# Performance work log

Hardware: AMD Instinct MI355X
Metric: run time of the kernel (lower is better)

The kernel has to match this reference:

```python
import jax, jax.numpy as jnp
import numpy as np
from jax import lax

MAX_INT = 10000.0
V, T0, E, H = 100000, 20, 256, 256
T = T0 + 2          # tagset_size + 2 (start = T-2, stop = T-1)
B, S = 32, 512
H2 = H // 2


def setup_inputs() -> dict:
    key = jax.random.key(0)
    ks = jax.random.split(key, 18)
    sd = 0.08
    trans = jax.random.normal(ks[0], (T, T), jnp.float32)
    trans = trans.at[-2, :].set(-MAX_INT).at[:, -1].set(-MAX_INT)
    return {
        "X": jax.random.randint(ks[1], (B, S), 0, V, jnp.int64),
        "Y": jax.random.randint(ks[2], (B, S), 0, T0, jnp.int64),
        "emb": jax.random.normal(ks[3], (V, E), jnp.float32) * sd,
        "Wih_f": jax.random.normal(ks[4], (4 * H2, E), jnp.float32) * sd,
        "Whh_f": jax.random.normal(ks[5], (4 * H2, H2), jnp.float32) * sd,
        "bih_f": jax.random.normal(ks[6], (4 * H2,), jnp.float32) * sd,
        "bhh_f": jax.random.normal(ks[7], (4 * H2,), jnp.float32) * sd,
        "Wih_b": jax.random.normal(ks[8], (4 * H2, E), jnp.float32) * sd,
        "Whh_b": jax.random.normal(ks[9], (4 * H2, H2), jnp.float32) * sd,
        "bih_b": jax.random.normal(ks[10], (4 * H2,), jnp.float32) * sd,
        "bhh_b": jax.random.normal(ks[11], (4 * H2,), jnp.float32) * sd,
        "fcW": jax.random.normal(ks[12], (T, H), jnp.float32) * sd,
        "fcb": jax.random.normal(ks[13], (T,), jnp.float32) * sd,
        "trans": trans,
        # original draws random (h0, c0) of shape (2, seq_len, H//2) each call
        "h0": jax.random.normal(ks[14], (2, S, H2), jnp.float32),
        "c0": jax.random.normal(ks[15], (2, S, H2), jnp.float32),
    }


def _lstm_dir(x, h0, c0, Wih, Whh, bih, bhh, reverse):
    # x: [B, S, E]; scans over axis 0 (as torch LSTM with batch_first=False does here)
    def step(carry, xt):
        h, c = carry
        g = xt @ Wih.T + bih + h @ Whh.T + bhh          # [S, 4*H2]
        i, f, gg, o = jnp.split(g, 4, axis=-1)
        c2 = jax.nn.sigmoid(f) * c + jax.nn.sigmoid(i) * jnp.tanh(gg)
        h2 = jax.nn.sigmoid(o) * jnp.tanh(c2)
        return (h2, c2), h2
    xs = x[::-1] if reverse else x
    _, hs = lax.scan(step, (h0, c0), xs)
    return hs[::-1] if reverse else hs                  # [B, S, H2]


def _feats(X, emb, Wih_f, Whh_f, bih_f, bhh_f, Wih_b, Whh_b, bih_b, bhh_b,
           fcW, fcb, h0, c0):
    e = emb[X]                                           # [B, S, E]
    hf = _lstm_dir(e, h0[0], c0[0], Wih_f, Whh_f, bih_f, bhh_f, False)
    hb = _lstm_dir(e, h0[1], c0[1], Wih_b, Whh_b, bih_b, bhh_b, True)
    lstm_out = jnp.concatenate([hf, hb], axis=-1)        # [B, S, H]
    return lstm_out @ fcW.T + fcb                        # [B, S, T]


def _crf_loss(feats, Y, trans):
    # forward algorithm (log partition), vectorized over batch
    alpha0 = jnp.full((B, T), -MAX_INT, feats.dtype).at[:, -2].set(0.0)

    def step(alpha, feat_t):                             # feat_t: [B, T]
        # alpha_new[b, next] = LSE_prev(alpha[b,prev] + trans[next,prev]) + feat[b,next]
        new = jax.nn.logsumexp(alpha[:, None, :] + trans[None, :, :], axis=2) + feat_t
        return new, None

    alpha, _ = lax.scan(step, alpha0, jnp.swapaxes(feats, 0, 1))
    forward_score = jax.nn.logsumexp(alpha + trans[-1][None, :], axis=1).mean()

    # gold score
    start = jnp.full((B, 1), T - 2, Y.dtype)
    tags = jnp.concatenate([start, Y], axis=1)           # [B, S+1]
    emit = jnp.take_along_axis(feats, Y[..., None], axis=2)[..., 0].sum(axis=1)
    trans_sc = trans[tags[:, 1:], tags[:, :-1]].sum(axis=1) + trans[-1, tags[:, -1]]
    gold_score = (emit + trans_sc).mean()
    return forward_score - gold_score


def reference(X, Y, emb, Wih_f, Whh_f, bih_f, bhh_f, Wih_b, Whh_b, bih_b, bhh_b,
              fcW, fcb, trans, h0, c0):
    feats = _feats(X, emb, Wih_f, Whh_f, bih_f, bhh_f, Wih_b, Whh_b, bih_b, bhh_b,
                   fcW, fcb, h0, c0)
    score = _crf_loss(feats, Y, trans)
    return score, Y
```

## Files before the change

kernel.cpp:

```cpp
#include <hip/hip_runtime.h>
#include <hip/hip_bf16.h>
#include <stdint.h>

typedef __attribute__((ext_vector_type(8))) short short8;
typedef __attribute__((ext_vector_type(4))) float f32x4;
typedef __attribute__((ext_vector_type(4))) unsigned short ushort4v;
typedef __attribute__((ext_vector_type(4))) unsigned int uint4v;

#define NB 32
#define NS 512
#define NE 256
#define NH2 128
#define NG 512
#define NT 22

__device__ __forceinline__ unsigned short f2bf(float f) {
    union { float f; unsigned u; } v; v.f = f;
    unsigned r = v.u + 0x7fffu + ((v.u >> 16) & 1u);
    return (unsigned short)(r >> 16);
}
__device__ __forceinline__ float bf2f(unsigned short b) {
    union { unsigned u; float f; } v; v.u = ((unsigned)b) << 16;
    return v.f;
}
__device__ __forceinline__ unsigned cvt_pk_bf16(float a, float b) {
    unsigned r;
    asm("v_cvt_pk_bf16_f32 %0, %1, %2" : "=v"(r) : "v"(a), "v"(b));
    return r;
}
__device__ __forceinline__ void wg_barrier() {
    __builtin_amdgcn_sched_barrier(0);
    asm volatile("s_waitcnt lgkmcnt(0)" ::: "memory");
    __builtin_amdgcn_s_barrier();
    __builtin_amdgcn_sched_barrier(0);
}
#define GL16(gsrc, ldst)                                                              \
    __builtin_amdgcn_global_load_lds(                                                 \
        (const __attribute__((address_space(1))) unsigned int*)(gsrc),                \
        (__attribute__((address_space(3))) unsigned int*)(ldst), 16, 0, 0)

__global__ void k_pre(const int* X, const float* emb, const int* Y,
                      const float* Wih_f, const float* Wih_b,
                      const float* Whh_f, const float* Whh_b, const float* fcW,
                      unsigned short* ebf, unsigned short* Wb_ih,
                      unsigned short* Wb_hh, unsigned short* fcpad, float* out,
                      unsigned* done_cnt)
{
    int idx = blockIdx.x * blockDim.x + threadIdx.x;
    if (idx == 0) *done_cnt = 0;
    const int nEmb = NB * NS * 64;
    if (idx < nEmb) {
        int r = idx >> 6, lane = idx & 63;
        int xr = X[r];
        f32x4 v = *(const f32x4*)(emb + (size_t)xr * NE + lane * 4);
        ushort4v o;
        o[0] = f2bf(v[0]); o[1] = f2bf(v[1]); o[2] = f2bf(v[2]); o[3] = f2bf(v[3]);
        *(ushort4v*)(ebf + (size_t)r * NE + lane * 4) = o;
        return;
    }
    int j = idx - nEmb;
    const int n1 = 2 * NG * NE;
    const int n2 = 2 * NG * NH2;
    const int n3 = 2 * 32 * NH2;
    const int n4 = NB * NS;
    if (j < n1) {
        const float* src = (j < NG * NE) ? Wih_f : Wih_b;
        Wb_ih[j] = f2bf(src[j % (NG * NE)]);
    } else if (j < n1 + n2) {
        int i2 = j - n1;
        const float* src = (i2 < NG * NH2) ? Whh_f : Whh_b;
        Wb_hh[i2] = f2bf(src[i2 % (NG * NH2)]);
    } else if (j < n1 + n2 + n3) {
        int i3 = j - n1 - n2;
        int d = i3 / (32 * NH2);
        int jj = (i3 / NH2) % 32;
        int k = i3 % NH2;
        fcpad[i3] = (jj < NT) ? f2bf(fcW[jj * 256 + d * NH2 + k]) : (unsigned short)0;
    } else if (j < n1 + n2 + n3 + n4) {
        int i4 = j - n1 - n2 - n3;
        out[1 + i4] = (float)Y[i4];
    }
}

__launch_bounds__(256)
__global__ void k_xproj(const unsigned short* ebf, const unsigned short* Wb_ih,
                        const float* bih_f, const float* bhh_f,
                        const float* bih_b, const float* bhh_b,
                        unsigned short* Xp)
{
    __shared__ __align__(16) unsigned short Atile[2][128 * 64];
    __shared__ __align__(16) unsigned short Btile[2][128 * 64];
    int dir = blockIdx.z;
    int r0 = blockIdx.x * 128;
    int g0 = blockIdx.y * 128;
    int tid = threadIdx.x;
    int w = tid >> 6, lane = tid & 63;
    int wr = w >> 1, wc = w & 1;
    int lrow = lane & 15, kg = lane >> 4;
    int srow8 = lane >> 3, schunk = lane & 7;
    const float* bih = dir ? bih_b : bih_f;
    const float* bhh = dir ? bhh_b : bhh_f;
    const unsigned short* Bsrc = Wb_ih + ((size_t)dir * NG + g0) * NE;
    const unsigned short* Asrc = ebf + (size_t)r0 * NE;

#define STAGE(bufi, ks)                                                                \
    do {                                                                               \
        int k0_ = (ks) * 64;                                                           \
        _Pragma("unroll")                                                              \
        for (int i_ = 0; i_ < 4; ++i_) {                                               \
            int rr_ = (w * 4 + i_) * 8 + srow8;                                        \
            GL16(Asrc + (size_t)rr_ * NE + k0_ + schunk * 8, &Atile[bufi][(w * 4 + i_) * 512]); \
            GL16(Bsrc + (size_t)rr_ * NE + k0_ + schunk * 8, &Btile[bufi][(w * 4 + i_) * 512]); \
        }                                                                              \
    } while (0)

    STAGE(0, 0);
    f32x4 acc[4][4] = {};
#pragma unroll
    for (int ks = 0; ks < 4; ++ks) {
        const int cur = ks & 1;
        if (ks < 3) {
            STAGE(cur ^ 1, ks + 1);
            asm volatile("s_waitcnt vmcnt(8)" ::: "memory");
        } else {
            asm volatile("s_waitcnt vmcnt(0)" ::: "memory");
        }
        __builtin_amdgcn_sched_barrier(0);
        __builtin_amdgcn_s_barrier();
        __builtin_amdgcn_sched_barrier(0);
        short8 a[4][2], b[4][2];
#pragma unroll
        for (int mi = 0; mi < 4; ++mi)
#pragma unroll
            for (int kk = 0; kk < 2; ++kk)
                a[mi][kk] = *(const short8*)&Atile[cur][(wr * 64 + mi * 16 + lrow) * 64 + kk * 32 + kg * 8];
#pragma unroll
        for (int ni = 0; ni < 4; ++ni)
#pragma unroll
            for (int kk = 0; kk < 2; ++kk)
                b[ni][kk] = *(const short8*)&Btile[cur][(wc * 64 + ni * 16 + lrow) * 64 + kk * 32 + kg * 8];
#pragma unroll
        for (int mi = 0; mi < 4; ++mi)
#pragma unroll
            for (int ni = 0; ni < 4; ++ni)
#pragma unroll
                for (int kk = 0; kk < 2; ++kk)
                    acc[mi][ni] = __builtin_amdgcn_mfma_f32_16x16x32_bf16(a[mi][kk], b[ni][kk], acc[mi][ni], 0, 0, 0);
        asm volatile("s_waitcnt lgkmcnt(0)" ::: "memory");
        __builtin_amdgcn_sched_barrier(0);
        __builtin_amdgcn_s_barrier();
        __builtin_amdgcn_sched_barrier(0);
    }
#undef STAGE

#pragma unroll
    for (int ni = 0; ni < 4; ++ni) {
        int g = g0 + wc * 64 + ni * 16 + lrow;
        float bias = bih[g] + bhh[g];
#pragma unroll
        for (int mi = 0; mi < 4; ++mi) {
            int r = r0 + wr * 64 + mi * 16 + kg * 4;
            int t = r >> 9;
            int s = r & 511;
            int sb = s >> 4;
            unsigned short* dst = Xp + ((((size_t)dir * 32 + sb) * 32 + t) << 13) + g * 16 + (s & 15);
            unsigned o0 = f2bf(acc[mi][ni][0] + bias);
            unsigned o1 = f2bf(acc[mi][ni][1] + bias);
            unsigned o2 = f2bf(acc[mi][ni][2] + bias);
            unsigned o3 = f2bf(acc[mi][ni][3] + bias);
            uint2 pk; pk.x = o0 | (o1 << 16); pk.y = o2 | (o3 << 16);
            *(uint2*)dst = pk;
        }
    }
}

__launch_bounds__(512, 2)
__global__ void k_lstm(const unsigned short* Wb_hh, const unsigned short* fcpad,
                       const unsigned short* Xp, const float* h0, const float* c0,
                       unsigned short* featsP)
{
    __shared__ unsigned short h_lds[2][16 * 136];
    __shared__ unsigned short featsL[512 * 24];
    int dir = blockIdx.x >> 5;
    int sb = blockIdx.x & 31;
    int s0 = sb * 16;
    int tid = threadIdx.x;
    int w = tid >> 6, lane = tid & 63;
    int lrow = lane & 15, kg = lane >> 4;

    short8 bfr[4][4];
#pragma unroll
    for (int q = 0; q < 4; ++q) {
        const unsigned short* p = Wb_hh + ((size_t)dir * NG + (q * 128 + w * 16 + lrow)) * NH2 + kg * 8;
#pragma unroll
        for (int kf = 0; kf < 4; ++kf)
            bfr[q][kf] = *(const short8*)(p + kf * 32);
    }
    short8 fcfr[4];
    if (w < 2) {
        const unsigned short* p = fcpad + ((size_t)dir * 32 + (w * 16 + lrow)) * NH2 + kg * 8;
#pragma unroll
        for (int kf = 0; kf < 4; ++kf)
            fcfr[kf] = *(const short8*)(p + kf * 32);
    }

    float c[4], ho[4];
#pragma unroll
    for (int i = 0; i < 4; ++i)
        c[i] = c0[((size_t)dir * NS + s0 + kg * 4 + i) * NH2 + w * 16 + lrow];
    {
        int sl = tid >> 5, hq = tid & 31;
        f32x4 hv = *(const f32x4*)(h0 + ((size_t)dir * NS + s0 + sl) * NH2 + hq * 4);
        ushort4v hb; hb[0] = f2bf(hv[0]); hb[1] = f2bf(hv[1]); hb[2] = f2bf(hv[2]); hb[3] = f2bf(hv[3]);
        *(ushort4v*)&h_lds[0][sl * 136 + hq * 4] = hb;
    }

    const unsigned short* xbase = Xp + (((size_t)dir * 32 + sb) * 32) * 8192;
    int xoff0 = (w * 16 + lrow) * 16 + kg * 4;
    ushort4v xA[4], xB[4];
#pragma unroll
    for (int q = 0; q < 4; ++q)
        xA[q] = *(const ushort4v*)(xbase + (size_t)(dir ? 31 : 0) * 8192 + xoff0 + q * 2048);
#pragma unroll
    for (int q = 0; q < 4; ++q)
        xB[q] = *(const ushort4v*)(xbase + (size_t)(dir ? 30 : 1) * 8192 + xoff0 + q * 2048);
    __syncthreads();

#define LSTM_STEP(T, XV, PR, PW)                                                       \
    {                                                                                  \
        short8 afr[4];                                                                 \
        _Pragma("unroll")                                                              \
        for (int kf = 0; kf < 4; ++kf)                                                 \
            afr[kf] = *(const short8*)&h_lds[PR][lrow * 136 + kf * 32 + kg * 8];       \
        f32x4 accA[4], accB[4];                                                        \
        _Pragma("unroll")                                                              \
        for (int q = 0; q < 4; ++q) {                                                  \
            f32x4 ci_;                                                                 \
            ci_[0] = bf2f(XV[q][0]); ci_[1] = bf2f(XV[q][1]);                          \
            ci_[2] = bf2f(XV[q][2]); ci_[3] = bf2f(XV[q][3]);                          \
            accA[q] = __builtin_amdgcn_mfma_f32_16x16x32_bf16(afr[0], bfr[q][0], ci_, 0, 0, 0); \
            f32x4 z_ = {};                                                             \
            accB[q] = __builtin_amdgcn_mfma_f32_16x16x32_bf16(afr[2], bfr[q][2], z_, 0, 0, 0);  \
        }                                                                              \
        _Pragma("unroll")                                                              \
        for (int q = 0; q < 4; ++q) {                                                  \
            accA[q] = __builtin_amdgcn_mfma_f32_16x16x32_bf16(afr[1], bfr[q][1], accA[q], 0, 0, 0); \
            accB[q] = __builtin_amdgcn_mfma_f32_16x16x32_bf16(afr[3], bfr[q][3], accB[q], 0, 0, 0); \
        }                                                                              \
        if (w < 2 && (T) > 0) {                    \
            int txp_ = dir ? 32 - (T) : (T) - 1;                                       \
            f32x4 fa_ = {};                                                            \
            _Pragma("unroll")                                                          \
            for (int kf = 0; kf < 4; ++kf)                                             \
                fa_ = __builtin_amdgcn_mfma_f32_16x16x32_bf16(afr[kf], fcfr[kf], fa_, 0, 0, 0); \
            int tag_ = w * 16 + lrow;                                                  \
            if (tag_ < NT) {                                                           \
                unsigned r01_ = cvt_pk_bf16(fa_[0], fa_[1]);                           \
                unsigned r23_ = cvt_pk_bf16(fa_[2], fa_[3]);                           \
                int rb_ = (txp_ * 16 + kg * 4) * 24 + tag_;                            \
                featsL[rb_]      = (unsigned short)r01_;                               \
                featsL[rb_ + 24] = (unsigned short)(r01_ >> 16);                       \
                featsL[rb_ + 48] = (unsigned short)r23_;                               \
                featsL[rb_ + 72] = (unsigned short)(r23_ >> 16);                       \
            }                                                                          \
        }                                                                              \
        if ((T) + 2 < 32) {                                                            \
            int txn = dir ? 29 - (T) : (T) + 2;                                        \
            _Pragma("unroll")                                                          \
            for (int q = 0; q < 4; ++q)                                                \
                XV[q] = *(const ushort4v*)(xbase + (size_t)txn * 8192 + xoff0 + q * 2048); \
        }                                                                              \
        _Pragma("unroll")                                                              \
        for (int i = 0; i < 4; ++i) {                                                  \
            float gi_ = accA[0][i] + accB[0][i];                                       \
            float gf_ = accA[1][i] + accB[1][i];                                       \
            float gg_ = accA[2][i] + accB[2][i];                                       \
            float go_ = accA[3][i] + accB[3][i];                                       \
            float ef_ = __expf(-gf_);                                                  \
            float sfc_ = c[i] * __builtin_amdgcn_rcpf(1.f + ef_);                      \
            float eg2_ = __expf(2.f * gg_);                                            \
            float ei_ = __expf(-gi_);                                                  \
            float tgsi_ = (eg2_ - 1.f) * __builtin_amdgcn_rcpf((1.f + ei_) * (eg2_ + 1.f)); \
            float cn_ = sfc_ + tgsi_;                                                  \
            c[i] = cn_;                                                                \
            float ec2_ = __expf(2.f * cn_);                                            \
            float eo_ = __expf(-go_);                                                  \
            ho[i] = (ec2_ - 1.f) * __builtin_amdgcn_rcpf((1.f + eo_) * (ec2_ + 1.f));  \
        }                                                                              \
        {                                                                              \
            unsigned r01_ = cvt_pk_bf16(ho[0], ho[1]);                                 \
            unsigned r23_ = cvt_pk_bf16(ho[2], ho[3]);                                 \
            int hb_ = (kg * 4) * 136 + w * 16 + lrow;                                  \
            h_lds[PW][hb_]       = (unsigned short)r01_;                               \
            h_lds[PW][hb_ + 136] = (unsigned short)(r01_ >> 16);                       \
            h_lds[PW][hb_ + 272] = (unsigned short)r23_;                               \
            h_lds[PW][hb_ + 408] = (unsigned short)(r23_ >> 16);                       \
        }                                                                              \
        wg_barrier();                                                                  \
    }

    for (int tt = 0; tt < 16; ++tt) {
        LSTM_STEP(2 * tt,     xA, ((2 * tt) & 1),     (((2 * tt) & 1) ^ 1))
        LSTM_STEP(2 * tt + 1, xB, ((2 * tt + 1) & 1), (((2 * tt + 1) & 1) ^ 1))
    }
#undef LSTM_STEP

    if (w < 2) {
        short8 afr[4];
#pragma unroll
        for (int kf = 0; kf < 4; ++kf)
            afr[kf] = *(const short8*)&h_lds[0][lrow * 136 + kf * 32 + kg * 8];
        f32x4 fa = {};
#pragma unroll
        for (int kf = 0; kf < 4; ++kf)
            fa = __builtin_amdgcn_mfma_f32_16x16x32_bf16(afr[kf], fcfr[kf], fa, 0, 0, 0);
        int txl = dir ? 0 : 31;
        int tag = w * 16 + lrow;
        if (tag < NT) {
            unsigned r01 = cvt_pk_bf16(fa[0], fa[1]);
            unsigned r23 = cvt_pk_bf16(fa[2], fa[3]);
            int rb = (txl * 16 + kg * 4) * 24 + tag;
            featsL[rb]      = (unsigned short)r01;
            featsL[rb + 24] = (unsigned short)(r01 >> 16);
            featsL[rb + 48] = (unsigned short)r23;
            featsL[rb + 72] = (unsigned short)(r23 >> 16);
        }
    }
    __syncthreads();
    int ftx = tid >> 4, fs = tid & 15;
    unsigned short* gdst = featsP + (((size_t)dir * 32 + ftx) * 512 + s0 + fs) * 24;
    const unsigned short* lsrc = featsL + (ftx * 16 + fs) * 24;
#pragma unroll
    for (int j = 0; j < 3; ++j)
        ((uint4v*)gdst)[j] = ((const uint4v*)lsrc)[j];
}

__device__ __forceinline__ float mm_combine(const unsigned short* Rb, const unsigned short* Tb,
                                            int lane, f32x4 c[2][2])
{
    int lrow = lane & 15, kg = lane >> 4;
    short8 a0 = *(const short8*)(Rb + lrow * 32 + kg * 8);
    short8 a1 = *(const short8*)(Rb + (16 + lrow) * 32 + kg * 8);
    short8 b0 = *(const short8*)(Tb + lrow * 32 + kg * 8);
    short8 b1 = *(const short8*)(Tb + (16 + lrow) * 32 + kg * 8);
    c[0][0] = __builtin_amdgcn_mfma_f32_16x16x32_bf16(a0, b0, c[0][0], 0, 0, 0);
    c[0][1] = __builtin_amdgcn_mfma_f32_16x16x32_bf16(a0, b1, c[0][1], 0, 0, 0);
    c[1][0] = __builtin_amdgcn_mfma_f32_16x16x32_bf16(a1, b0, c[1][0], 0, 0, 0);
    c[1][1] = __builtin_amdgcn_mfma_f32_16x16x32_bf16(a1, b1, c[1][1], 0, 0, 0);
    float mx = 0.f;
#pragma unroll
    for (int ti = 0; ti < 2; ++ti)
#pragma unroll
        for (int tj = 0; tj < 2; ++tj)
#pragma unroll
            for (int i = 0; i < 4; ++i) mx = fmaxf(mx, c[ti][tj][i]);
#pragma unroll
    for (int off = 32; off; off >>= 1) mx = fmaxf(mx, __shfl_xor(mx, off));
    return fmaxf(mx, 1e-30f);
}

__device__ __forceinline__ void write_scaled(unsigned short* outp, bool Rlayout,
                                             int lane, const f32x4 c[2][2], float inv)
{
    int lrow = lane & 15, kg = lane >> 4;
    if (Rlayout) {
#pragma unroll
        for (int ti = 0; ti < 2; ++ti)
#pragma unroll
            for (int tj = 0; tj < 2; ++tj) {
                int cc = tj * 16 + lrow;
#pragma unroll
                for (int i = 0; i < 4; ++i) {
                    int r = ti * 16 + kg * 4 + i;
                    float v = (r < NT && cc < NT) ? c[ti][tj][i] * inv : 0.f;
                    outp[r * 32 + cc] = f2bf(v);
                }
            }
    } else {
#pragma unroll
        for (int ti = 0; ti < 2; ++ti)
#pragma unroll
            for (int tj = 0; tj < 2; ++tj) {
                int cc = tj * 16 + lrow;
                int r0 = ti * 16 + kg * 4;
                ushort4v pk;
#pragma unroll
                for (int i = 0; i < 4; ++i) {
                    int r = r0 + i;
                    float v = (r < NT && cc < NT) ? c[ti][tj][i] * inv : 0.f;
                    pk[i] = f2bf(v);
                }
                *(ushort4v*)(outp + cc * 32 + r0) = pk;
            }
    }
}

__launch_bounds__(256)
__global__ void k_fcrf(const unsigned short* featsP, const float* fcb, const float* trans,
                       const int* Y, unsigned short* Mseg, float* lscseg, float* goldp)
{
    __shared__ unsigned short mats[16 * 1024];
    __shared__ float etR[484], etT[484];
    __shared__ float ef[16 * 24];
    __shared__ float fl[16 * 24];
    __shared__ float lscm[16];
    int b = blockIdx.x, seg = blockIdx.y;
    int tid = threadIdx.x;
    int w = tid >> 6, lane = tid & 63;

    for (int i = tid; i < 484; i += 256) {
        float e = __expf(trans[i]);
        etR[i] = e;
        etT[(i % NT) * NT + (i / NT)] = e;
    }
    for (int i = tid; i < 16 * NT; i += 256) {
        int s = i / NT, j = i % NT;
        size_t base = ((size_t)b * 512 + seg * 16 + s) * 24 + j;
        float f = bf2f(featsP[base]) + bf2f(featsP[(size_t)32 * 512 * 24 + base]) + fcb[j];
        fl[s * 24 + j] = f;
        ef[s * 24 + j] = __expf(f);
    }
    if (tid < 16) lscm[tid] = 0.f;
    __syncthreads();

    if (w == 3 && lane < 16) {
        int sg = seg * 16 + lane;
        int y = Y[b * NS + sg];
        int yp = sg ? Y[b * NS + sg - 1] : (NT - 2);
        float gp = fl[lane * 24 + y] + trans[y * NT + yp];
#pragma unroll
        for (int off = 8; off; off >>= 1) gp += __shfl_xor(gp, off);
        if (lane == 0) goldp[b * 32 + seg] = gp;
    }

    for (int u = tid; u < 16 * 512; u += 256) {
        int t = u >> 9, cell2 = u & 511, row = cell2 >> 4, col = (cell2 & 15) * 2;
        float v0 = 0.f, v1 = 0.f;
        if (row < NT) {
            if (t & 1) {
                if (col < NT)     v0 = etR[row * NT + col]     * ef[t * 24 + row];
                if (col + 1 < NT) v1 = etR[row * NT + col + 1] * ef[t * 24 + row];
            } else {
                if (col < NT)     v0 = etT[row * NT + col]     * ef[t * 24 + col];
                if (col + 1 < NT) v1 = etT[row * NT + col + 1] * ef[t * 24 + col + 1];
            }
        }
        ((unsigned*)mats)[u] = (unsigned)f2bf(v0) | ((unsigned)f2bf(v1) << 16);
    }
    __syncthreads();

    for (int lvl = 0; lvl < 4; ++lvl) {
        int nP = 8 >> lvl;
        for (int p = w; p < nP; p += 4) {
            int aslot = (2 * p) << lvl, bslot = (2 * p + 1) << lvl;
            f32x4 c[2][2] = {};
            float mx = mm_combine(mats + bslot * 1024, mats + aslot * 1024, lane, c);
            float inv = __builtin_amdgcn_rcpf(mx);
            float nlsc = lscm[aslot] + lscm[bslot] + __logf(mx);
            if (lvl < 3) {
                write_scaled(mats + aslot * 1024, (p & 1) != 0, lane, c, inv);
                if (lane == 0) lscm[aslot] = nlsc;
            } else {
                write_scaled(Mseg + ((size_t)b * 32 + seg) * 1024, (seg & 1) != 0, lane, c, inv);
                if (lane == 0) lscseg[b * 32 + seg] = nlsc;
            }
        }
        __syncthreads();
    }
}

__launch_bounds__(256)
__global__ void k_crf2(const unsigned short* Mseg, const float* lscseg,
                       const float* trans, const int* Y, const float* goldp,
                       float* fwd_sc, float* gold_sc, unsigned* done_cnt, float* out)
{
    __shared__ unsigned short mats[16 * 1024];
    __shared__ float lscm[16];
    __shared__ float tl[484];
    __shared__ float col20[32];
    __shared__ unsigned lastflag;
    int b = blockIdx.x;
    int tid = threadIdx.x;
    int w = tid >> 6, lane = tid & 63;
    int lrow = lane & 15, kg = lane >> 4;

    for (int i = tid; i < 484; i += 256) tl[i] = trans[i];
    __syncthreads();

    const unsigned short* base = Mseg + (size_t)b * 32 * 1024;
    for (int p = w; p < 16; p += 4) {
        f32x4 c[2][2] = {};
        float mx = mm_combine(base + (2 * p + 1) * 1024, base + (2 * p) * 1024, lane, c);
        float inv = __builtin_amdgcn_rcpf(mx);
        float nlsc = lscseg[b * 32 + 2 * p] + lscseg[b * 32 + 2 * p + 1] + __logf(mx);
        write_scaled(mats + p * 1024, (p & 1) != 0, lane, c, inv);
        if (lane == 0) lscm[p] = nlsc;
    }
    __syncthreads();

    for (int lvl = 0; lvl < 4; ++lvl) {
        int nP = 8 >> lvl;
        for (int p = w; p < nP; p += 4) {
            int aslot = (2 * p) << lvl, bslot = (2 * p + 1) << lvl;
            f32x4 c[2][2] = {};
            float mx = mm_combine(mats + bslot * 1024, mats + aslot * 1024, lane, c);
            if (lvl < 3) {
                float inv = __builtin_amdgcn_rcpf(mx);
                float nlsc = lscm[aslot] + lscm[bslot] + __logf(mx);
                write_scaled(mats + aslot * 1024, (p & 1) != 0, lane, c, inv);
                if (lane == 0) lscm[aslot] = nlsc;
            } else {
                if (lrow == 4) {
#pragma unroll
                    for (int ti = 0; ti < 2; ++ti)
#pragma unroll
                        for (int i = 0; i < 4; ++i)
                            col20[ti * 16 + kg * 4 + i] = c[ti][1][i];
                }
                if (lane == 0) lscm[0] = lscm[0] + lscm[8];
            }
        }
        __syncthreads();
    }

    if (w == 0) {
        float v = 0.f;
        if (lane < NT) v = __expf(tl[(NT - 1) * NT + lane]) * col20[lane];
#pragma unroll
        for (int off = 32; off; off >>= 1) v += __shfl_xor(v, off);
        if (lane == 0) fwd_sc[b] = __logf(v) + lscm[0];
    }
    if (w == 1) {
        float g = (lane < 32) ? goldp[b * 32 + lane] : 0.f;
#pragma unroll
        for (int off = 16; off; off >>= 1) g += __shfl_xor(g, off);
        if (lane == 0) gold_sc[b] = g + tl[(NT - 1) * NT + Y[b * NS + NS - 1]];
    }
    __syncthreads();
    if (tid == 0) {
        __threadfence();
        lastflag = (atomicAdd(done_cnt, 1u) == 31u) ? 1u : 0u;
    }
    __syncthreads();
    if (lastflag && w == 0) {
        __threadfence();
        float v = (lane < NB) ? (fwd_sc[lane] - gold_sc[lane]) : 0.f;
#pragma unroll
        for (int off = 32; off; off >>= 1) v += __shfl_xor(v, off);
        if (lane == 0) out[0] = v * (1.f / NB);
    }
}

extern "C" void kernel_launch(void* const* d_in, const int* in_sizes, int n_in,
                              void* d_out, int out_size, void* d_ws, size_t ws_size,
                              hipStream_t stream)
{
    const int* X = (const int*)d_in[0];
    const int* Y = (const int*)d_in[1];
    const float* emb = (const float*)d_in[2];
    const float* Wih_f = (const float*)d_in[3];
    const float* Whh_f = (const float*)d_in[4];
    const float* bih_f = (const float*)d_in[5];
    const float* bhh_f = (const float*)d_in[6];
    const float* Wih_b = (const float*)d_in[7];
    const float* Whh_b = (const float*)d_in[8];
    const float* bih_b = (const float*)d_in[9];
    const float* bhh_b = (const float*)d_in[10];
    const float* fcW = (const float*)d_in[11];
    const float* fcb = (const float*)d_in[12];
    const float* trans = (const float*)d_in[13];
    const float* h0 = (const float*)d_in[14];
    const float* c0 = (const float*)d_in[15];
    float* out = (float*)d_out;

    char* ws = (char*)d_ws;
    unsigned short* Wb_ih  = (unsigned short*)(ws + 0);
    unsigned short* Wb_hh  = (unsigned short*)(ws + 524288);
    unsigned short* fcpad  = (unsigned short*)(ws + 786432);
    unsigned short* Xp     = (unsigned short*)(ws + 802816);
    unsigned short* featsP = (unsigned short*)(ws + 34357248);
    float* goldp           = (float*)(ws + 35930112);
    float* fwd_sc          = (float*)(ws + 35934208);
    float* gold_sc         = (float*)(ws + 35934336);
    unsigned* done_cnt     = (unsigned*)(ws + 35934464);
    unsigned short* ebf    = (unsigned short*)(ws + 35934592);
    unsigned short* Mseg   = ebf;
    float* lscseg          = (float*)(ws + 44323200);

    k_pre<<<dim3(5728), dim3(256), 0, stream>>>(X, emb, Y, Wih_f, Wih_b, Whh_f, Whh_b,
                                                fcW, ebf, Wb_ih, Wb_hh, fcpad, out, done_cnt);
    k_xproj<<<dim3(128, 4, 2), dim3(256), 0, stream>>>(ebf, Wb_ih, bih_f, bhh_f, bih_b, bhh_b, Xp);
    k_lstm<<<dim3(64), dim3(512), 0, stream>>>(Wb_hh, fcpad, Xp, h0, c0, featsP);
    k_fcrf<<<dim3(32, 32), dim3(256), 0, stream>>>(featsP, fcb, trans, Y, Mseg, lscseg, goldp);
    k_crf2<<<dim3(NB), dim3(256), 0, stream>>>(Mseg, lscseg, trans, Y, goldp,
                                               fwd_sc, gold_sc, done_cnt, out);
    (void)in_sizes; (void)n_in; (void)out_size; (void)ws_size;
}
```

Before: 93.67 us.

## Merge LSTM directions into one 1024-thread block and store feats directly

The LSTM kernel now runs both directions of each 16-sequence slice in a single 1024-thread workgroup (32 blocks instead of 64), with a per-direction h buffer in LDS. The LDS staging of the emission features is removed, and each step writes scalar bf16 values straight to global memory. This halves the number of workgroups and frees LDS, but the per-step barrier now synchronises 16 waves instead of 8, and the global feature stores become scattered 2-byte writes.

```diff
diff --git a/kernel.cpp b/kernel.cpp
--- a/kernel.cpp
+++ b/kernel.cpp
@@ -174,31 +174,31 @@
     }
 }
 
-__launch_bounds__(512, 2)
+__launch_bounds__(1024, 1)
 __global__ void k_lstm(const unsigned short* Wb_hh, const unsigned short* fcpad,
                        const unsigned short* Xp, const float* h0, const float* c0,
                        unsigned short* featsP)
 {
-    __shared__ unsigned short h_lds[2][16 * 136];
-    __shared__ unsigned short featsL[512 * 24];
-    int dir = blockIdx.x >> 5;
-    int sb = blockIdx.x & 31;
+    __shared__ unsigned short h_lds[2][2][16 * 136];
+    int sb = blockIdx.x;
     int s0 = sb * 16;
     int tid = threadIdx.x;
     int w = tid >> 6, lane = tid & 63;
+    int dirv = w >> 3;
+    int wl = w & 7;
     int lrow = lane & 15, kg = lane >> 4;
 
     short8 bfr[4][4];
 #pragma unroll
     for (int q = 0; q < 4; ++q) {
-        const unsigned short* p = Wb_hh + ((size_t)dir * NG + (q * 128 + w * 16 + lrow)) * NH2 + kg * 8;
+        const unsigned short* p = Wb_hh + ((size_t)dirv * NG + (q * 128 + wl * 16 + lrow)) * NH2 + kg * 8;
 #pragma unroll
         for (int kf = 0; kf < 4; ++kf)
             bfr[q][kf] = *(const short8*)(p + kf * 32);
     }
     short8 fcfr[4];
-    if (w < 2) {
-        const unsigned short* p = fcpad + ((size_t)dir * 32 + (w * 16 + lrow)) * NH2 + kg * 8;
+    if (wl < 2) {
+        const unsigned short* p = fcpad + ((size_t)dirv * 32 + (wl * 16 + lrow)) * NH2 + kg * 8;
 #pragma unroll
         for (int kf = 0; kf < 4; ++kf)
             fcfr[kf] = *(const short8*)(p + kf * 32);
@@ -207,23 +207,24 @@
     float c[4], ho[4];
 #pragma unroll
     for (int i = 0; i < 4; ++i)
-        c[i] = c0[((size_t)dir * NS + s0 + kg * 4 + i) * NH2 + w * 16 + lrow];
+        c[i] = c0[((size_t)dirv * NS + s0 + kg * 4 + i) * NH2 + wl * 16 + lrow];
     {
-        int sl = tid >> 5, hq = tid & 31;
-        f32x4 hv = *(const f32x4*)(h0 + ((size_t)dir * NS + s0 + sl) * NH2 + hq * 4);
+        int tidh = tid & 511;
+        int sl = tidh >> 5, hq = tidh & 31;
+        f32x4 hv = *(const f32x4*)(h0 + ((size_t)dirv * NS + s0 + sl) * NH2 + hq * 4);
         ushort4v hb; hb[0] = f2bf(hv[0]); hb[1] = f2bf(hv[1]); hb[2] = f2bf(hv[2]); hb[3] = f2bf(hv[3]);
-        *(ushort4v*)&h_lds[0][sl * 136 + hq * 4] = hb;
-    }
-
-    const unsigned short* xbase = Xp + (((size_t)dir * 32 + sb) * 32) * 8192;
-    int xoff0 = (w * 16 + lrow) * 16 + kg * 4;
+        *(ushort4v*)&h_lds[dirv][0][sl * 136 + hq * 4] = hb;
+    }
+
+    const unsigned short* xbase = Xp + (((size_t)dirv * 32 + sb) * 32) * 8192;
+    int xoff0 = (wl * 16 + lrow) * 16 + kg * 4;
     ushort4v xA[4], xB[4];
 #pragma unroll
     for (int q = 0; q < 4; ++q)
-        xA[q] = *(const ushort4v*)(xbase + (size_t)(dir ? 31 : 0) * 8192 + xoff0 + q * 2048);
+        xA[q] = *(const ushort4v*)(xbase + (size_t)(dirv ? 31 : 0) * 8192 + xoff0 + q * 2048);
 #pragma unroll
     for (int q = 0; q < 4; ++q)
-        xB[q] = *(const ushort4v*)(xbase + (size_t)(dir ? 30 : 1) * 8192 + xoff0 + q * 2048);
+        xB[q] = *(const ushort4v*)(xbase + (size_t)(dirv ? 30 : 1) * 8192 + xoff0 + q * 2048);
     __syncthreads();
 
 #define LSTM_STEP(T, XV, PR, PW)                                                       \
@@ -231,7 +232,7 @@
         short8 afr[4];                                                                 \
         _Pragma("unroll")                                                              \
         for (int kf = 0; kf < 4; ++kf)                                                 \
-            afr[kf] = *(const short8*)&h_lds[PR][lrow * 136 + kf * 32 + kg * 8];       \
+            afr[kf] = *(const short8*)&h_lds[dirv][PR][lrow * 136 + kf * 32 + kg * 8]; \
         f32x4 accA[4], accB[4];                                                        \
         _Pragma("unroll")                                                              \
         for (int q = 0; q < 4; ++q) {                                                  \
@@ -247,25 +248,21 @@
             accA[q] = __builtin_amdgcn_mfma_f32_16x16x32_bf16(afr[1], bfr[q][1], accA[q], 0, 0, 0); \
             accB[q] = __builtin_amdgcn_mfma_f32_16x16x32_bf16(afr[3], bfr[q][3], accB[q], 0, 0, 0); \
         }                                                                              \
-        if (w < 2 && (T) > 0) {                    \
-            int txp_ = dir ? 32 - (T) : (T) - 1;                                       \
+        if (wl < 2 && (T) > 0) {         \
+            int txp_ = dirv ? 32 - (T) : (T) - 1;                                      \
             f32x4 fa_ = {};                                                            \
             _Pragma("unroll")                                                          \
             for (int kf = 0; kf < 4; ++kf)                                             \
                 fa_ = __builtin_amdgcn_mfma_f32_16x16x32_bf16(afr[kf], fcfr[kf], fa_, 0, 0, 0); \
-            int tag_ = w * 16 + lrow;                                                  \
+            int tag_ = wl * 16 + lrow;                                                 \
             if (tag_ < NT) {                                                           \
-                unsigned r01_ = cvt_pk_bf16(fa_[0], fa_[1]);                           \
-                unsigned r23_ = cvt_pk_bf16(fa_[2], fa_[3]);                           \
-                int rb_ = (txp_ * 16 + kg * 4) * 24 + tag_;                            \
-                featsL[rb_]      = (unsigned short)r01_;                               \
-                featsL[rb_ + 24] = (unsigned short)(r01_ >> 16);                       \
-                featsL[rb_ + 48] = (unsigned short)r23_;                               \
-                featsL[rb_ + 72] = (unsigned short)(r23_ >> 16);                       \
+                _Pragma("unroll")                                                      \
+                for (int i = 0; i < 4; ++i)                                            \
+                    featsP[(((size_t)dirv * 32 + txp_) * 512 + s0 + kg * 4 + i) * 24 + tag_] = f2bf(fa_[i]); \
             }                                                                          \
         }                                                                              \
         if ((T) + 2 < 32) {                                                            \
-            int txn = dir ? 29 - (T) : (T) + 2;                                        \
+            int txn = dirv ? 29 - (T) : (T) + 2;                                       \
             _Pragma("unroll")                                                          \
             for (int q = 0; q < 4; ++q)                                                \
                 XV[q] = *(const ushort4v*)(xbase + (size_t)txn * 8192 + xoff0 + q * 2048); \
@@ -290,11 +287,11 @@
         {                                                                              \
             unsigned r01_ = cvt_pk_bf16(ho[0], ho[1]);                                 \
             unsigned r23_ = cvt_pk_bf16(ho[2], ho[3]);                                 \
-            int hb_ = (kg * 4) * 136 + w * 16 + lrow;                                  \
-            h_lds[PW][hb_]       = (unsigned short)r01_;                               \
-            h_lds[PW][hb_ + 136] = (unsigned short)(r01_ >> 16);                       \
-            h_lds[PW][hb_ + 272] = (unsigned short)r23_;                               \
-            h_lds[PW][hb_ + 408] = (unsigned short)(r23_ >> 16);                       \
+            int hb_ = (kg * 4) * 136 + wl * 16 + lrow;                                 \
+            h_lds[dirv][PW][hb_]       = (unsigned short)r01_;                         \
+            h_lds[dirv][PW][hb_ + 136] = (unsigned short)(r01_ >> 16);                 \
+            h_lds[dirv][PW][hb_ + 272] = (unsigned short)r23_;                         \
+            h_lds[dirv][PW][hb_ + 408] = (unsigned short)(r23_ >> 16);                 \
         }                                                                              \
         wg_barrier();                                                                  \
     }
@@ -305,34 +302,23 @@
     }
 #undef LSTM_STEP
 
-    if (w < 2) {
+    if (wl < 2) {
         short8 afr[4];
 #pragma unroll
         for (int kf = 0; kf < 4; ++kf)
-            afr[kf] = *(const short8*)&h_lds[0][lrow * 136 + kf * 32 + kg * 8];
+            afr[kf] = *(const short8*)&h_lds[dirv][0][lrow * 136 + kf * 32 + kg * 8];
         f32x4 fa = {};
 #pragma unroll
         for (int kf = 0; kf < 4; ++kf)
             fa = __builtin_amdgcn_mfma_f32_16x16x32_bf16(afr[kf], fcfr[kf], fa, 0, 0, 0);
-        int txl = dir ? 0 : 31;
-        int tag = w * 16 + lrow;
+        int txl = dirv ? 0 : 31;
+        int tag = wl * 16 + lrow;
         if (tag < NT) {
-            unsigned r01 = cvt_pk_bf16(fa[0], fa[1]);
-            unsigned r23 = cvt_pk_bf16(fa[2], fa[3]);
-            int rb = (txl * 16 + kg * 4) * 24 + tag;
-            featsL[rb]      = (unsigned short)r01;
-            featsL[rb + 24] = (unsigned short)(r01 >> 16);
-            featsL[rb + 48] = (unsigned short)r23;
-            featsL[rb + 72] = (unsigned short)(r23 >> 16);
+#pragma unroll
+            for (int i = 0; i < 4; ++i)
+                featsP[(((size_t)dirv * 32 + txl) * 512 + s0 + kg * 4 + i) * 24 + tag] = f2bf(fa[i]);
         }
     }
-    __syncthreads();
-    int ftx = tid >> 4, fs = tid & 15;
-    unsigned short* gdst = featsP + (((size_t)dir * 32 + ftx) * 512 + s0 + fs) * 24;
-    const unsigned short* lsrc = featsL + (ftx * 16 + fs) * 24;
-#pragma unroll
-    for (int j = 0; j < 3; ++j)
-        ((uint4v*)gdst)[j] = ((const uint4v*)lsrc)[j];
 }
 
 __device__ __forceinline__ float mm_combine(const unsigned short* Rb, const unsigned short* Tb,
@@ -590,7 +576,7 @@
     k_pre<<<dim3(5728), dim3(256), 0, stream>>>(X, emb, Y, Wih_f, Wih_b, Whh_f, Whh_b,
                                                 fcW, ebf, Wb_ih, Wb_hh, fcpad, out, done_cnt);
     k_xproj<<<dim3(128, 4, 2), dim3(256), 0, stream>>>(ebf, Wb_ih, bih_f, bhh_f, bih_b, bhh_b, Xp);
-    k_lstm<<<dim3(64), dim3(512), 0, stream>>>(Wb_hh, fcpad, Xp, h0, c0, featsP);
+    k_lstm<<<dim3(32), dim3(1024), 0, stream>>>(Wb_hh, fcpad, Xp, h0, c0, featsP);
     k_fcrf<<<dim3(32, 32), dim3(256), 0, stream>>>(featsP, fcb, trans, Y, Mseg, lscseg, goldp);
     k_crf2<<<dim3(NB), dim3(256), 0, stream>>>(Mseg, lscseg, trans, Y, goldp,
                                                fwd_sc, gold_sc, done_cnt, out);
```

Measured after the change: 229.6 us. 145% more time.
